# Optimization experiments

Hardware: AMD Instinct MI355X
Metric: run time of the kernel (lower is better)

Reference implementation:

```python
import jax, jax.numpy as jnp
import numpy as np

B, S, D, N = 4, 1024, 1024, 32768


def setup_inputs() -> dict:
    key = jax.random.key(0)
    ks = jax.random.split(key, 6)
    return {
        "x": jax.random.normal(ks[0], (B, S, D), jnp.float32),
        "h": jax.random.normal(ks[1], (B, S, D), jnp.float32),
        "emb": jax.random.normal(ks[2], (N, D), jnp.float32),
        "tau_offset": jax.random.normal(ks[3], (B, S, 1), jnp.float32) * 0.1,
        "w_read": jax.random.normal(ks[4], (N, D), jnp.float32) * 0.02,
        "w_write": jax.random.normal(ks[5], (N, D), jnp.float32) * 0.02,
        "n_chunks": 8,
    }


def _srw_chunked(x, h, emb_unit, tau_offset, w_read, w_write, n_chunks):
    """Two chunked passes over neuron pool: (1) online score stats, (2) STE
    threshold-gated read->write projection with cost-weighted normalization."""
    Bb, Ss, Dd = x.shape
    Nn = emb_unit.shape[0]
    cs = Nn // n_chunks
    h_bf = h.astype(jnp.bfloat16)
    x_bf = x.astype(jnp.bfloat16)
    emb_bf = emb_unit.astype(jnp.bfloat16)
    read_bf = w_read.astype(jnp.bfloat16)
    write_bf = w_write.astype(jnp.bfloat16)
    z1 = jnp.zeros((Bb, Ss, 1))

    @jax.checkpoint
    def stats_step(carry, i):
        s_sum, sq_sum, ns_sum, ns_sq = carry
        s = i * cs
        ec = jax.lax.dynamic_slice_in_dim(emb_bf, s, cs, axis=0)
        scores = h_bf @ ec.T  # [B,S,cs]
        s_sum = s_sum + scores.sum(axis=-1, keepdims=True).astype(jnp.float32)
        sq_sum = sq_sum + (scores.astype(jnp.float32) ** 2).sum(axis=-1, keepdims=True)
        per_neuron_score = scores.astype(jnp.float32).mean(axis=(0, 1))
        ns_sum = ns_sum + per_neuron_score.sum()
        ns_sq = ns_sq + (per_neuron_score ** 2).sum()
        return ((s_sum, sq_sum, ns_sum, ns_sq), None)

    z_bs1 = jnp.zeros((Bb, Ss, 1))
    z_scalar = jnp.float32(0.0)
    (s_sum, sq_sum, ns_sum, ns_sq), _ = jax.lax.scan(
        stats_step, (z_bs1, z_bs1, z_scalar, z_scalar), jnp.arange(n_chunks))
    s_mean = s_sum / Nn
    s_std = jnp.sqrt(sq_sum / Nn - s_mean ** 2) + 1e-08
    tau = s_mean + tau_offset * s_std
    mean_score = ns_sum / Nn
    var_score = ns_sq / Nn - mean_score ** 2
    score_lb = var_score / (mean_score ** 2 + var_score + 0.01)

    @jax.checkpoint
    def gate_srw_step(carry, i):
        out, total_weighted_cost, total_gate_max, total_active = carry
        s = i * cs
        ec = jax.lax.dynamic_slice_in_dim(emb_bf, s, cs, axis=0)
        rc = jax.lax.dynamic_slice_in_dim(read_bf, s, cs, axis=0)
        wc = jax.lax.dynamic_slice_in_dim(write_bf, s, cs, axis=0)
        rc = rc / (jnp.linalg.norm(rc, axis=-1, keepdims=True) + 1e-08)
        wc = wc / (jnp.linalg.norm(wc, axis=-1, keepdims=True) + 1e-08)
        scores = h_bf @ ec.T
        raw = scores.astype(jnp.float32) - tau
        gate_hard = (raw > 0).astype(jnp.float32)
        sig = jax.nn.sigmoid(raw / s_std)
        gate = gate_hard + sig - jax.lax.stop_gradient(sig)  # straight-through
        gate_bf = gate.astype(jnp.bfloat16)
        xr = x_bf @ rc.T                     # read projection [B,S,cs]
        c_out = (gate_bf * xr @ wc).astype(jnp.float32)  # write projection
        xr_f32 = xr.astype(jnp.float32)
        cost = jax.lax.stop_gradient(xr_f32 ** 2)
        chunk_weighted = (sig * cost).sum(axis=-1, keepdims=True)
        chunk_active = gate_hard.sum(axis=-1, keepdims=True)
        return ((out + c_out,
                 total_weighted_cost + chunk_weighted,
                 jnp.maximum(total_gate_max, gate_hard.max(axis=-1, keepdims=True)),
                 total_active + chunk_active), None)

    (raw_out, total_weighted_cost, total_gate_max, total_active), _ = jax.lax.scan(
        gate_srw_step,
        (jnp.zeros((Bb, Ss, Dd), dtype=jnp.float32), z1,
         jnp.full((Bb, Ss, 1), -1000000000.0), z1),
        jnp.arange(n_chunks))
    den = jnp.sqrt(total_weighted_cost + 1e-06)
    den = jnp.maximum(den, 0.001)
    out = (raw_out / den).astype(jnp.bfloat16)
    score_std_out = s_std.mean()
    es_out = total_weighted_cost.mean()
    active_n_mean = total_active.mean()
    score_mean_out = s_mean.mean()
    return (out.astype(jnp.float32), total_active / Nn, total_gate_max, score_lb,
            score_std_out, es_out, active_n_mean, score_mean_out)


def reference(x, h, emb, tau_offset, w_read, w_write, n_chunks):
    # Caller normalizes the embedding pool to unit rows before the chunked pass.
    emb_unit = emb / (jnp.linalg.norm(emb, axis=-1, keepdims=True) + 1e-08)
    return _srw_chunked(x, h, emb_unit, tau_offset, w_read, w_write, n_chunks)
```

## Files before the change

### kernel.cpp

```cpp
#include <hip/hip_runtime.h>
#include <stdint.h>

#define M_TOT 4096
#define D_DIM 1024
#define N_NEUR 32768
#define NCHUNK 8
#define CS 4096

typedef float f32x4 __attribute__((ext_vector_type(4)));
typedef __bf16 bf16x8 __attribute__((ext_vector_type(8)));
typedef unsigned short u16;
typedef unsigned int u32;
typedef u16 u16x8 __attribute__((ext_vector_type(8)));
typedef u16 u16x4 __attribute__((ext_vector_type(4)));

__device__ __forceinline__ u16 f2bf(float f) {
    u32 u = __builtin_bit_cast(u32, f);
    u = (u + 0x7FFFu + ((u >> 16) & 1u)) >> 16;
    return (u16)u;
}
__device__ __forceinline__ float bf2f(u16 h) {
    u32 u = ((u32)h) << 16;
    return __builtin_bit_cast(float, u);
}
__device__ __forceinline__ u32 pack2(float a, float b, float s) {
    return (u32)f2bf(a * s) | ((u32)f2bf(b * s) << 16);
}

typedef __attribute__((address_space(1))) const u32 as1_u32;
typedef __attribute__((address_space(3))) u32 as3_u32;
__device__ __forceinline__ void gload16(const void* g, void* l) {
    __builtin_amdgcn_global_load_lds((as1_u32*)g, (as3_u32*)l, 16, 0, 0);
}

#define MFMA(a, b, c) __builtin_amdgcn_mfma_f32_16x16x32_bf16((a), (b), (c), 0, 0, 0)

#define GEMM128_BODY(ABASE, ASTR, BBASE, BSTR, KLEN)                                  \
    __shared__ u16 LDS[17408];                                                        \
    u16* Al = LDS;                                                                    \
    u16* Bl = LDS + 4096;                                                             \
    const int t = threadIdx.x, lane = t & 63, w = t >> 6;                             \
    const int wr = w >> 1, wc = w & 1, l15 = lane & 15, lg = lane >> 4;               \
    f32x4 acc[4][4] = {};                                                             \
    {                                                                                 \
        const int rb = lane >> 2, cl = (lane & 3) * 8;                                \
        const int seg0 = w * 2;                                                       \
        const size_t ro0 = (size_t)(seg0 * 16 + rb);                                  \
        const u16* pa0 = (ABASE) + ((size_t)bm * 128 + ro0) * (ASTR) + cl;            \
        const u16* pb0 = (BBASE) + ((size_t)bn * 128 + ro0) * (BSTR) + cl;            \
        const u16* pa1 = pa0 + (size_t)16 * (ASTR);                                   \
        const u16* pb1 = pb0 + (size_t)16 * (BSTR);                                   \
        u16* la0 = Al + seg0 * 512;                                                   \
        u16* lb0 = Bl + seg0 * 512;                                                   \
        for (int k0 = 0; k0 < (KLEN); k0 += 32) {                                     \
            __syncthreads();                                                          \
            gload16(pa0 + k0, la0);                                                   \
            gload16(pa1 + k0, la0 + 512);                                             \
            gload16(pb0 + k0, lb0);                                                   \
            gload16(pb1 + k0, lb0 + 512);                                             \
            __syncthreads();                                                          \
            bf16x8 afr[4], bfr[4];                                                    \
            _Pragma("unroll") for (int m = 0; m < 4; m++)                             \
                afr[m] = *(const bf16x8*)&Al[(wr * 64 + m * 16 + l15) * 32 + lg * 8]; \
            _Pragma("unroll") for (int n = 0; n < 4; n++)                             \
                bfr[n] = *(const bf16x8*)&Bl[(wc * 64 + n * 16 + l15) * 32 + lg * 8]; \
            _Pragma("unroll") for (int m = 0; m < 4; m++)                             \
                _Pragma("unroll") for (int n = 0; n < 4; n++)                         \
                    acc[m][n] = MFMA(afr[m], bfr[n], acc[m][n]);                      \
        }                                                                             \
    }

#define RESTAGE_TO_LDS(VALS)                                                          \
    __syncthreads();                                                                  \
    _Pragma("unroll") for (int m = 0; m < 4; m++)                                     \
        _Pragma("unroll") for (int rr = 0; rr < 4; rr++)                              \
            _Pragma("unroll") for (int n = 0; n < 4; n++) {                           \
                int lrow = wr * 64 + m * 16 + lg * 4 + rr;                            \
                LDS[lrow * 136 + wc * 64 + n * 16 + l15] = (VALS);                    \
            }                                                                         \
    __syncthreads();

#define RESTAGE_U16_TILE(VALS, DSTBASE, DSTSTRIDE, COLBASE)                           \
    {                                                                                 \
        RESTAGE_TO_LDS(VALS)                                                          \
        int row_ = t >> 2, c0_ = (t & 3) * 32;                                        \
        _Pragma("unroll") for (int p = 0; p < 2; p++) {                               \
            int lrow = p * 64 + row_;                                                 \
            u16* dst_ = (DSTBASE) + (size_t)(bm * 128 + lrow) * (DSTSTRIDE) +         \
                        (COLBASE) + c0_;                                              \
            const u16* srcl_ = &LDS[lrow * 136 + c0_];                                \
            _Pragma("unroll") for (int j = 0; j < 4; j++)                             \
                *(u16x8*)(dst_ + j * 8) = *(const u16x8*)(srcl_ + j * 8);             \
        }                                                                             \
    }

__global__ __launch_bounds__(256) void k_cvt(const float* __restrict__ h,
                                             const float* __restrict__ x,
                                             u16* __restrict__ hb, u16* __restrict__ xb) {
    size_t i = ((size_t)blockIdx.x * 256 + threadIdx.x) * 4;
    float4 v = *(const float4*)(h + i);
    uint2 o;
    o.x = pack2(v.x, v.y, 1.0f);
    o.y = pack2(v.z, v.w, 1.0f);
    *(uint2*)(hb + i) = o;
    v = *(const float4*)(x + i);
    o.x = pack2(v.x, v.y, 1.0f);
    o.y = pack2(v.z, v.w, 1.0f);
    *(uint2*)(xb + i) = o;
}

__global__ __launch_bounds__(256) void k_cvt_ern3(const float* __restrict__ emb,
                                                  const float* __restrict__ wrd,
                                                  const float* __restrict__ ww,
                                                  u16* __restrict__ ebf, u16* __restrict__ rbf,
                                                  float* __restrict__ sw) {
    int t = threadIdx.x, lane = t & 63, wv = t >> 6;
    int row = blockIdx.x * 4 + wv;
    int which = blockIdx.y;
    const float* srcm = which == 0 ? emb : (which == 1 ? wrd : ww);
    const float4* src = (const float4*)(srcm + (size_t)row * D_DIM);
    float4 v[4];
    float ss = 0.f;
#pragma unroll
    for (int j = 0; j < 4; j++) {
        v[j] = src[j * 64 + lane];
        if (which == 0) {
            ss += v[j].x * v[j].x + v[j].y * v[j].y + v[j].z * v[j].z + v[j].w * v[j].w;
        } else {
            float a = bf2f(f2bf(v[j].x)), b = bf2f(f2bf(v[j].y));
            float c = bf2f(f2bf(v[j].z)), d = bf2f(f2bf(v[j].w));
            ss += a * a + b * b + c * c + d * d;
        }
    }
#pragma unroll
    for (int s = 1; s < 64; s <<= 1) ss += __shfl_xor(ss, s);
    float sc = 1.0f / (sqrtf(ss) + 1e-8f);
    if (which == 2) {
        if (lane == 0) sw[row] = sc;
        return;
    }
    uint2* dst = (uint2*)((which == 0 ? ebf : rbf) + (size_t)row * D_DIM);
#pragma unroll
    for (int j = 0; j < 4; j++) {
        uint2 o;
        o.x = pack2(v[j].x, v[j].y, sc);
        o.y = pack2(v[j].z, v[j].w, sc);
        dst[j * 64 + lane] = o;
    }
}

__global__ __launch_bounds__(256) void k_cvt_e_norm(const float* __restrict__ emb,
                                                    int cbase, u16* __restrict__ ebf) {
    int t = threadIdx.x, lane = t & 63, wv = t >> 6;
    int row = blockIdx.x * 4 + wv;
    const float4* src = (const float4*)(emb + (size_t)(cbase + row) * D_DIM);
    float4 v[4];
    float ss = 0.f;
#pragma unroll
    for (int j = 0; j < 4; j++) {
        v[j] = src[j * 64 + lane];
        ss += v[j].x * v[j].x + v[j].y * v[j].y + v[j].z * v[j].z + v[j].w * v[j].w;
    }
#pragma unroll
    for (int s = 1; s < 64; s <<= 1) ss += __shfl_xor(ss, s);
    float es = 1.0f / (sqrtf(ss) + 1e-8f);
    uint2* dst = (uint2*)(ebf + (size_t)row * D_DIM);
#pragma unroll
    for (int j = 0; j < 4; j++) {
        uint2 o;
        o.x = pack2(v[j].x, v[j].y, es);
        o.y = pack2(v[j].z, v[j].w, es);
        dst[j * 64 + lane] = o;
    }
}

__global__ __launch_bounds__(256) void k_cvt_r_norm(const float* __restrict__ wrd,
                                                    int cbase, u16* __restrict__ rbf) {
    int t = threadIdx.x, lane = t & 63, wv = t >> 6;
    int row = blockIdx.x * 4 + wv;
    const float4* src = (const float4*)(wrd + (size_t)(cbase + row) * D_DIM);
    float4 v[4];
    float ss = 0.f;
#pragma unroll
    for (int j = 0; j < 4; j++) {
        v[j] = src[j * 64 + lane];
        float a = bf2f(f2bf(v[j].x)), b = bf2f(f2bf(v[j].y));
        float c = bf2f(f2bf(v[j].z)), d = bf2f(f2bf(v[j].w));
        ss += a * a + b * b + c * c + d * d;
    }
#pragma unroll
    for (int s = 1; s < 64; s <<= 1) ss += __shfl_xor(ss, s);
    float rs = 1.0f / (sqrtf(ss) + 1e-8f);
    uint2* dst = (uint2*)(rbf + (size_t)row * D_DIM);
#pragma unroll
    for (int j = 0; j < 4; j++) {
        uint2 o;
        o.x = pack2(v[j].x, v[j].y, rs);
        o.y = pack2(v[j].z, v[j].w, rs);
        dst[j * 64 + lane] = o;
    }
}

__global__ __launch_bounds__(256) void k_sw(const float* __restrict__ ww, float* sw) {
    int t = threadIdx.x, lane = t & 63, wv = t >> 6;
    int row = blockIdx.x * 4 + wv;
    const float4* src = (const float4*)(ww + (size_t)row * D_DIM);
    float ss = 0.f;
#pragma unroll
    for (int j = 0; j < 4; j++) {
        float4 v = src[j * 64 + lane];
        float a = bf2f(f2bf(v.x)), b = bf2f(f2bf(v.y));
        float c = bf2f(f2bf(v.z)), d = bf2f(f2bf(v.w));
        ss += a * a + b * b + c * c + d * d;
    }
#pragma unroll
    for (int s = 1; s < 64; s <<= 1) ss += __shfl_xor(ss, s);
    if (lane == 0) sw[row] = 1.0f / (sqrtf(ss) + 1e-8f);
}

__global__ __launch_bounds__(256) void k_tww(const float* __restrict__ ww,
                                             const float* __restrict__ sw,
                                             int cbase, u16* __restrict__ wwT, int dstr) {
    __shared__ u16 tile[64][80];
    int kt = blockIdx.x * 64;
    int dt = blockIdx.y * 64;
    int t = threadIdx.x;
    int kk = t >> 4;
    int dd = (t & 15) * 4;
#pragma unroll
    for (int i = 0; i < 4; i++) {
        int krow = kk + i * 16;
        int kg = cbase + kt + krow;
        float s = sw[kg];
        float4 v = *(const float4*)(ww + (size_t)kg * D_DIM + dt + dd);
        tile[dd + 0][krow] = f2bf(v.x * s);
        tile[dd + 1][krow] = f2bf(v.y * s);
        tile[dd + 2][krow] = f2bf(v.z * s);
        tile[dd + 3][krow] = f2bf(v.w * s);
    }
    __syncthreads();
    int dd2 = t >> 2;
    int kk2 = (t & 3) * 16;
    uint4 o0 = *(const uint4*)&tile[dd2][kk2];
    uint4 o1 = *(const uint4*)&tile[dd2][kk2 + 8];
    u16* dst = wwT + (size_t)(dt + dd2) * dstr + kt + kk2;
    *(uint4*)dst = o0;
    *(uint4*)(dst + 8) = o1;
}

__global__ __launch_bounds__(256) void k_pass1(const u16* __restrict__ hb,
                                               const u16* __restrict__ ebf, int cbase,
                                               float* rowsum, float* rowsq, float* colsum,
                                               u16* __restrict__ sb, int sstr) {
    int bm = blockIdx.x, bn = blockIdx.y;
    GEMM128_BODY(hb, D_DIM, ebf, D_DIM, D_DIM)
    float csv[4] = {0.f, 0.f, 0.f, 0.f};
#pragma unroll
    for (int m = 0; m < 4; m++)
#pragma unroll
        for (int rr = 0; rr < 4; rr++)
#pragma unroll
            for (int n = 0; n < 4; n++) csv[n] += bf2f(f2bf(acc[m][n][rr]));
#pragma unroll
    for (int n = 0; n < 4; n++) {
        float cv = csv[n];
        cv += __shfl_xor(cv, 16);
        cv += __shfl_xor(cv, 32);
        if (lg == 0) {
            int ng = cbase + bn * 128 + wc * 64 + n * 16 + l15;
            atomicAdd(&colsum[ng], cv);
        }
    }
    RESTAGE_TO_LDS(f2bf(acc[m][n][rr]))
    int row_ = t >> 2, c0_ = (t & 3) * 32;
#pragma unroll
    for (int p = 0; p < 2; p++) {
        int lrow = p * 64 + row_;
        int grow = bm * 128 + lrow;
        float rs = 0.f, rq = 0.f;
        u16* dst = sb ? (sb + (size_t)grow * sstr + cbase + bn * 128 + c0_) : (u16*)nullptr;
#pragma unroll
        for (int j = 0; j < 4; j++) {
            u16x8 v = *(const u16x8*)&LDS[lrow * 136 + c0_ + j * 8];
            if (dst) *(u16x8*)(dst + j * 8) = v;
#pragma unroll
            for (int q = 0; q < 8; q++) {
                float sv = bf2f(v[q]);
                rs += sv;
                rq += sv * sv;
            }
        }
        rs += __shfl_xor(rs, 1);
        rq += __shfl_xor(rq, 1);
        rs += __shfl_xor(rs, 2);
        rq += __shfl_xor(rq, 2);
        if ((lane & 3) == 0) {
            atomicAdd(&rowsum[grow], rs);
            atomicAdd(&rowsq[grow], rq);
        }
    }
}

__global__ __launch_bounds__(256) void k_ns(const float* __restrict__ colsum, float* scal) {
    int i = blockIdx.x * 256 + threadIdx.x;
    float pm = colsum[i] * (1.0f / 4096.0f);
    float s1 = pm, s2 = pm * pm;
#pragma unroll
    for (int x = 1; x < 64; x <<= 1) {
        s1 += __shfl_xor(s1, x);
        s2 += __shfl_xor(s2, x);
    }
    __shared__ float sh[2][4];
    int w = threadIdx.x >> 6;
    if ((threadIdx.x & 63) == 0) { sh[0][w] = s1; sh[1][w] = s2; }
    __syncthreads();
    if (threadIdx.x == 0) {
        atomicAdd(&scal[0], sh[0][0] + sh[0][1] + sh[0][2] + sh[0][3]);
        atomicAdd(&scal[1], sh[1][0] + sh[1][1] + sh[1][2] + sh[1][3]);
    }
}

__global__ __launch_bounds__(256) void k_tau(const float* __restrict__ rowsum,
                                             const float* __restrict__ rowsq,
                                             const float* __restrict__ tau_off,
                                             float* tau, float* invstd, float* smean, float* sstd) {
    int i = blockIdx.x * 256 + threadIdx.x;
    float sm = rowsum[i] * (1.0f / 32768.0f);
    float var = rowsq[i] * (1.0f / 32768.0f) - sm * sm;
    float sd = sqrtf(var) + 1e-8f;
    smean[i] = sm;
    sstd[i] = sd;
    invstd[i] = 1.0f / sd;
    tau[i] = sm + tau_off[i] * sd;
}

__global__ __launch_bounds__(256) void k_xr_gate_all(const u16* __restrict__ xb,
                                                     const u16* __restrict__ rbf,
                                                     u16* __restrict__ sbP,
                                                     const float* __restrict__ tau,
                                                     const float* __restrict__ invstd,
                                                     float* twc, float* act) {
    int bm = blockIdx.x, bn = blockIdx.y;
    const int tt = threadIdx.x;
    const int prow = tt >> 2, pc0 = (tt & 3) * 32;
    u16x8 sv_pre[2][4];
#pragma unroll
    for (int p = 0; p < 2; p++) {
        int grow = bm * 128 + p * 64 + prow;
        const u16* src = sbP + (size_t)grow * N_NEUR + bn * 128 + pc0;
#pragma unroll
        for (int j = 0; j < 4; j++) sv_pre[p][j] = *(const u16x8*)(src + j * 8);
    }
    GEMM128_BODY(xb, D_DIM, rbf, D_DIM, D_DIM)
    RESTAGE_TO_LDS(f2bf(acc[m][n][rr]))
#pragma unroll
    for (int p = 0; p < 2; p++) {
        int lrow = p * 64 + prow;
        int grow = bm * 128 + lrow;
        float tl = tau[grow], il = invstd[grow];
        float wsum = 0.f, cnt = 0.f;
        u16* gptr = sbP + (size_t)grow * N_NEUR + bn * 128 + pc0;
#pragma unroll
        for (int j = 0; j < 4; j++) {
            u16x8 xr8 = *(const u16x8*)&LDS[lrow * 136 + pc0 + j * 8];
            u16x8 sv8 = sv_pre[p][j];
            u16x8 o;
#pragma unroll
            for (int q = 0; q < 8; q++) {
                float xf = bf2f(xr8[q]);
                float raw = bf2f(sv8[q]) - tl;
                float sig = 1.0f / (1.0f + __expf(-raw * il));
                bool g = raw > 0.0f;
                wsum += sig * xf * xf;
                cnt += g ? 1.0f : 0.0f;
                o[q] = g ? xr8[q] : (u16)0;
            }
            *(u16x8*)(gptr + j * 8) = o;
        }
        wsum += __shfl_xor(wsum, 1);
        cnt += __shfl_xor(cnt, 1);
        wsum += __shfl_xor(wsum, 2);
        cnt += __shfl_xor(cnt, 2);
        if ((lane & 3) == 0) {
            atomicAdd(&twc[grow], wsum);
            atomicAdd(&act[grow], cnt);
        }
    }
}

__global__ __launch_bounds__(256) void k_pass2b_all(const u16* __restrict__ sbP,
                                                    const u16* __restrict__ wwT,
                                                    u16* __restrict__ part) {
    int bm = blockIdx.x;
    int bn = blockIdx.y;
    int zz = blockIdx.z;
    const u16* Pz = sbP + (size_t)zz * CS;
    const u16* Wz = wwT + (size_t)zz * CS;
    u16* pz = part + (size_t)zz * M_TOT * D_DIM;
    GEMM128_BODY(Pz, N_NEUR, Wz, N_NEUR, CS)
    RESTAGE_U16_TILE(f2bf(acc[m][n][rr]), pz, D_DIM, bn * 128)
}

__global__ __launch_bounds__(256) void k_norm_comb(const u16* __restrict__ part,
                                                   const float* __restrict__ twc,
                                                   const float* __restrict__ act,
                                                   float* __restrict__ out0,
                                                   float* out1, float* out2) {
    int row = blockIdx.x;
    float den = sqrtf(twc[row] + 1e-6f);
    den = fmaxf(den, 0.001f);
    float inv = 1.0f / den;
    size_t base = (size_t)row * D_DIM + threadIdx.x * 4;
    float s0 = 0.f, s1 = 0.f, s2 = 0.f, s3 = 0.f;
#pragma unroll
    for (int c = 0; c < NCHUNK; c++) {
        u16x4 v = *(const u16x4*)(part + (size_t)c * M_TOT * D_DIM + base);
        s0 += bf2f(v[0]);
        s1 += bf2f(v[1]);
        s2 += bf2f(v[2]);
        s3 += bf2f(v[3]);
    }
    float4 o;
    o.x = bf2f(f2bf(s0 * inv));
    o.y = bf2f(f2bf(s1 * inv));
    o.z = bf2f(f2bf(s2 * inv));
    o.w = bf2f(f2bf(s3 * inv));
    *(float4*)(out0 + base) = o;
    if (threadIdx.x == 0) {
        out1[row] = act[row] * (1.0f / 32768.0f);
        out2[row] = act[row] > 0.0f ? 1.0f : 0.0f;
    }
}

__global__ __launch_bounds__(256) void k_xr_plain(const u16* __restrict__ xb,
                                                  const u16* __restrict__ rbf,
                                                  u16* __restrict__ P) {
    int bm = blockIdx.x, bn = blockIdx.y;
    GEMM128_BODY(xb, D_DIM, rbf, D_DIM, D_DIM)
    RESTAGE_U16_TILE(f2bf(acc[m][n][rr]), P, CS, bn * 128)
}

__global__ __launch_bounds__(256) void k_gate_gemm(const u16* __restrict__ hb,
                                                   const u16* __restrict__ ebf,
                                                   const float* __restrict__ tau,
                                                   const float* __restrict__ invstd,
                                                   u16* __restrict__ P, float* twc, float* act) {
    int bm = blockIdx.x, bn = blockIdx.y;
    GEMM128_BODY(hb, D_DIM, ebf, D_DIM, D_DIM)
#pragma unroll
    for (int m = 0; m < 4; m++) {
#pragma unroll
        for (int rr = 0; rr < 4; rr++) {
            int mg = bm * 128 + wr * 64 + m * 16 + lg * 4 + rr;
            float tl = tau[mg], il = invstd[mg];
            float wsum = 0.f, cnt = 0.f;
#pragma unroll
            for (int n = 0; n < 4; n++) {
                int ngl = bn * 128 + wc * 64 + n * 16 + l15;
                float sv = bf2f(f2bf(acc[m][n][rr]));
                float raw = sv - tl;
                u16 xrb = P[(size_t)mg * CS + ngl];
                float xf = bf2f(xrb);
                float sig = 1.0f / (1.0f + __expf(-raw * il));
                bool g = raw > 0.0f;
                wsum += sig * xf * xf;
                cnt += g ? 1.0f : 0.0f;
                P[(size_t)mg * CS + ngl] = g ? xrb : (u16)0;
            }
#pragma unroll
            for (int x = 1; x < 16; x <<= 1) {
                wsum += __shfl_xor(wsum, x);
                cnt += __shfl_xor(cnt, x);
            }
            if (l15 == 0) {
                atomicAdd(&twc[mg], wsum);
                atomicAdd(&act[mg], cnt);
            }
        }
    }
}

__global__ __launch_bounds__(256) void k_pass2b(const u16* __restrict__ P,
                                                const u16* __restrict__ wwT, int bstr,
                                                float* __restrict__ out) {
    int bm = blockIdx.x;
    int bn = blockIdx.y;
    GEMM128_BODY(P, CS, wwT, bstr, CS)
#pragma unroll
    for (int m = 0; m < 4; m++)
#pragma unroll
        for (int n = 0; n < 4; n++)
#pragma unroll
            for (int rr = 0; rr < 4; rr++) {
                int mg = bm * 128 + wr * 64 + m * 16 + lg * 4 + rr;
                int dg = bn * 128 + wc * 64 + n * 16 + l15;
                out[(size_t)mg * D_DIM + dg] += bf2f(f2bf(acc[m][n][rr]));
            }
}

__global__ __launch_bounds__(256) void k_norm_f(float* __restrict__ out,
                                                const float* __restrict__ twc,
                                                const float* __restrict__ act,
                                                float* out1, float* out2) {
    int row = blockIdx.x;
    float den = sqrtf(twc[row] + 1e-6f);
    den = fmaxf(den, 0.001f);
    float inv = 1.0f / den;
    float* p = out + (size_t)row * D_DIM;
    int i = threadIdx.x * 4;
    float4 v = *(float4*)(p + i);
    v.x = bf2f(f2bf(v.x * inv));
    v.y = bf2f(f2bf(v.y * inv));
    v.z = bf2f(f2bf(v.z * inv));
    v.w = bf2f(f2bf(v.w * inv));
    *(float4*)(p + i) = v;
    if (threadIdx.x == 0) {
        out1[row] = act[row] * (1.0f / 32768.0f);
        out2[row] = act[row] > 0.0f ? 1.0f : 0.0f;
    }
}

__global__ __launch_bounds__(256) void k_scalars(const float* __restrict__ smean,
                                                 const float* __restrict__ sstd,
                                                 const float* __restrict__ twc,
                                                 const float* __restrict__ act,
                                                 const float* __restrict__ scal,
                                                 float* outS) {
    float a = 0.f, b = 0.f, c = 0.f, d = 0.f;
    for (int i = threadIdx.x; i < 4096; i += 256) {
        a += smean[i];
        b += sstd[i];
        c += twc[i];
        d += act[i];
    }
#pragma unroll
    for (int x = 1; x < 64; x <<= 1) {
        a += __shfl_xor(a, x);
        b += __shfl_xor(b, x);
        c += __shfl_xor(c, x);
        d += __shfl_xor(d, x);
    }
    __shared__ float sh[4][4];
    int w = threadIdx.x >> 6;
    if ((threadIdx.x & 63) == 0) { sh[0][w] = a; sh[1][w] = b; sh[2][w] = c; sh[3][w] = d; }
    __syncthreads();
    if (threadIdx.x == 0) {
        float ma = sh[0][0] + sh[0][1] + sh[0][2] + sh[0][3];
        float mb = sh[1][0] + sh[1][1] + sh[1][2] + sh[1][3];
        float mc = sh[2][0] + sh[2][1] + sh[2][2] + sh[2][3];
        float md = sh[3][0] + sh[3][1] + sh[3][2] + sh[3][3];
        float mean_score = scal[0] * (1.0f / 32768.0f);
        float var_score = scal[1] * (1.0f / 32768.0f) - mean_score * mean_score;
        outS[0] = var_score / (mean_score * mean_score + var_score + 0.01f);
        outS[1] = mb * (1.0f / 4096.0f);
        outS[2] = mc * (1.0f / 4096.0f);
        outS[3] = md * (1.0f / 4096.0f);
        outS[4] = ma * (1.0f / 4096.0f);
    }
}

static constexpr size_t OFF_HB     = 0;
static constexpr size_t OFF_XB     = 8388608;
static constexpr size_t OFF_P      = 16777216;
static constexpr size_t OFF_EBF    = 50331648;
static constexpr size_t OFF_RBF    = 117440512;
static constexpr size_t OFF_WWT    = 184549376;
static constexpr size_t OFF_SW     = 251658240;
static constexpr size_t OFF_ROWSUM = 251789312;
static constexpr size_t OFF_ROWSQ  = 251805696;
static constexpr size_t OFF_COLSUM = 251822080;
static constexpr size_t OFF_TAU    = 251953152;
static constexpr size_t OFF_INVSTD = 251969536;
static constexpr size_t OFF_SMEAN  = 251985920;
static constexpr size_t OFF_SSTD   = 252002304;
static constexpr size_t OFF_TWC    = 252018688;
static constexpr size_t OFF_ACT    = 252035072;
static constexpr size_t OFF_SCAL   = 252051456;
static constexpr size_t STATS_END  = 252051520;
static constexpr size_t ZERO_LEN   = STATS_END - OFF_ROWSUM;
static constexpr size_t OFF_SB     = 252706816;
static constexpr size_t FULL_END   = OFF_SB + (size_t)M_TOT * N_NEUR * 2;
static constexpr size_t OFF_PART   = OFF_EBF;

extern "C" void kernel_launch(void* const* d_in, const int* in_sizes, int n_in,
                              void* d_out, int out_size, void* d_ws, size_t ws_size,
                              hipStream_t stream) {
    const float* x = (const float*)d_in[0];
    const float* h = (const float*)d_in[1];
    const float* emb = (const float*)d_in[2];
    const float* tau_off = (const float*)d_in[3];
    const float* w_read = (const float*)d_in[4];
    const float* w_write = (const float*)d_in[5];
    char* ws = (char*)d_ws;
    u16* hb = (u16*)(ws + OFF_HB);
    u16* xb = (u16*)(ws + OFF_XB);
    u16* P = (u16*)(ws + OFF_P);
    u16* ebf = (u16*)(ws + OFF_EBF);
    u16* rbf = (u16*)(ws + OFF_RBF);
    u16* wwT = (u16*)(ws + OFF_WWT);
    float* sw = (float*)(ws + OFF_SW);
    float* rowsum = (float*)(ws + OFF_ROWSUM);
    float* rowsq = (float*)(ws + OFF_ROWSQ);
    float* colsum = (float*)(ws + OFF_COLSUM);
    float* tau = (float*)(ws + OFF_TAU);
    float* invstd = (float*)(ws + OFF_INVSTD);
    float* smean = (float*)(ws + OFF_SMEAN);
    float* sstd = (float*)(ws + OFF_SSTD);
    float* twc = (float*)(ws + OFF_TWC);
    float* act = (float*)(ws + OFF_ACT);
    float* scal = (float*)(ws + OFF_SCAL);
    u16* part = (u16*)(ws + OFF_PART);
    const bool fullA = ws_size >= FULL_END;
    u16* sbP = fullA ? (u16*)(ws + OFF_SB) : (u16*)nullptr;

    float* out0 = (float*)d_out;
    float* out1 = out0 + (size_t)M_TOT * D_DIM;
    float* out2 = out1 + M_TOT;
    float* outS = out2 + M_TOT;

    hipMemsetAsync(ws + OFF_ROWSUM, 0, ZERO_LEN, stream);

    k_cvt<<<4096, 256, 0, stream>>>(h, x, hb, xb);

    if (fullA) {
        k_cvt_ern3<<<dim3(N_NEUR / 4, 3), 256, 0, stream>>>(emb, w_read, w_write,
                                                            ebf, rbf, sw);
        k_tww<<<dim3(N_NEUR / 64, 16), 256, 0, stream>>>(w_write, sw, 0, wwT, N_NEUR);
        k_pass1<<<dim3(32, 256), 256, 0, stream>>>(hb, ebf, 0, rowsum, rowsq, colsum,
                                                   sbP, N_NEUR);
        k_ns<<<128, 256, 0, stream>>>(colsum, scal);
        k_tau<<<16, 256, 0, stream>>>(rowsum, rowsq, tau_off, tau, invstd, smean, sstd);
        k_xr_gate_all<<<dim3(32, 256), 256, 0, stream>>>(xb, rbf, sbP, tau, invstd, twc, act);
        k_pass2b_all<<<dim3(32, 8, 8), 256, 0, stream>>>(sbP, wwT, part);
        k_norm_comb<<<4096, 256, 0, stream>>>(part, twc, act, out0, out1, out2);
    } else {
        hipMemsetAsync(d_out, 0, (size_t)M_TOT * D_DIM * 4, stream);
        k_sw<<<N_NEUR / 4, 256, 0, stream>>>(w_write, sw);
        for (int c = 0; c < NCHUNK; c++) {
            k_cvt_e_norm<<<CS / 4, 256, 0, stream>>>(emb, c * CS, ebf);
            k_pass1<<<dim3(32, 32), 256, 0, stream>>>(hb, ebf, c * CS, rowsum, rowsq, colsum,
                                                      (u16*)nullptr, 0);
        }
        k_ns<<<128, 256, 0, stream>>>(colsum, scal);
        k_tau<<<16, 256, 0, stream>>>(rowsum, rowsq, tau_off, tau, invstd, smean, sstd);
        for (int c = 0; c < NCHUNK; c++) {
            k_cvt_e_norm<<<CS / 4, 256, 0, stream>>>(emb, c * CS, ebf);
            k_cvt_r_norm<<<CS / 4, 256, 0, stream>>>(w_read, c * CS, rbf);
            k_tww<<<dim3(CS / 64, 16), 256, 0, stream>>>(w_write, sw, c * CS, wwT, CS);
            k_xr_plain<<<dim3(32, 32), 256, 0, stream>>>(xb, rbf, P);
            k_gate_gemm<<<dim3(32, 32), 256, 0, stream>>>(hb, ebf, tau, invstd, P, twc, act);
            k_pass2b<<<dim3(32, 8), 256, 0, stream>>>(P, wwT, CS, out0);
        }
        k_norm_f<<<4096, 256, 0, stream>>>(out0, twc, act, out1, out2);
    }
    k_scalars<<<1, 256, 0, stream>>>(smean, sstd, twc, act, scal, outS);
}
```

Before: 1.509 ms.

## Double-buffer LDS tiles in GEMM main loop to overlap loads with MFMA

Splits the shared-memory staging area into two halves. The next K-slice is prefetched with global_load_lds while the current slice feeds the MFMAs, and explicit vmcnt waits plus raw s_barrier replace the two __syncthreads per iteration. The goal is to hide global-load latency behind compute in every GEMM built on this macro. The cost is reliance on hand-written waitcnt and barrier ordering, which could be fragile if the compiler reorders LDS reads.

```diff
diff --git a/kernel.cpp b/kernel.cpp
--- a/kernel.cpp
+++ b/kernel.cpp
@@ -37,36 +37,45 @@
 
 #define GEMM128_BODY(ABASE, ASTR, BBASE, BSTR, KLEN)                                  \
     __shared__ u16 LDS[17408];                                                        \
-    u16* Al = LDS;                                                                    \
-    u16* Bl = LDS + 4096;                                                             \
     const int t = threadIdx.x, lane = t & 63, w = t >> 6;                             \
     const int wr = w >> 1, wc = w & 1, l15 = lane & 15, lg = lane >> 4;               \
     f32x4 acc[4][4] = {};                                                             \
     {                                                                                 \
+        const int seg0 = w * 2;                                                       \
         const int rb = lane >> 2, cl = (lane & 3) * 8;                                \
-        const int seg0 = w * 2;                                                       \
         const size_t ro0 = (size_t)(seg0 * 16 + rb);                                  \
         const u16* pa0 = (ABASE) + ((size_t)bm * 128 + ro0) * (ASTR) + cl;            \
         const u16* pb0 = (BBASE) + ((size_t)bn * 128 + ro0) * (BSTR) + cl;            \
         const u16* pa1 = pa0 + (size_t)16 * (ASTR);                                   \
         const u16* pb1 = pb0 + (size_t)16 * (BSTR);                                   \
-        u16* la0 = Al + seg0 * 512;                                                   \
-        u16* lb0 = Bl + seg0 * 512;                                                   \
+        gload16(pa0, LDS + seg0 * 512);                                               \
+        gload16(pa1, LDS + seg0 * 512 + 512);                                         \
+        gload16(pb0, LDS + 4096 + seg0 * 512);                                        \
+        gload16(pb1, LDS + 4096 + seg0 * 512 + 512);                                  \
         for (int k0 = 0; k0 < (KLEN); k0 += 32) {                                     \
-            __syncthreads();                                                          \
-            gload16(pa0 + k0, la0);                                                   \
-            gload16(pa1 + k0, la0 + 512);                                             \
-            gload16(pb0 + k0, lb0);                                                   \
-            gload16(pb1 + k0, lb0 + 512);                                             \
-            __syncthreads();                                                          \
+            const int co = ((k0 >> 5) & 1) * 8192;                                    \
+            const int no = co ^ 8192;                                                 \
+            if (k0 + 32 < (KLEN)) {                                                   \
+                gload16(pa0 + k0 + 32, LDS + no + seg0 * 512);                        \
+                gload16(pa1 + k0 + 32, LDS + no + seg0 * 512 + 512);                  \
+                gload16(pb0 + k0 + 32, LDS + no + 4096 + seg0 * 512);                 \
+                gload16(pb1 + k0 + 32, LDS + no + 4096 + seg0 * 512 + 512);           \
+                asm volatile("s_waitcnt vmcnt(4)" ::: "memory");                      \
+            } else {                                                                  \
+                asm volatile("s_waitcnt vmcnt(0)" ::: "memory");                      \
+            }                                                                         \
+            __builtin_amdgcn_s_barrier();                                             \
             bf16x8 afr[4], bfr[4];                                                    \
             _Pragma("unroll") for (int m = 0; m < 4; m++)                             \
-                afr[m] = *(const bf16x8*)&Al[(wr * 64 + m * 16 + l15) * 32 + lg * 8]; \
+                afr[m] = *(const bf16x8*)&LDS[co + (wr * 64 + m * 16 + l15) * 32 +    \
+                                              lg * 8];                                \
             _Pragma("unroll") for (int n = 0; n < 4; n++)                             \
-                bfr[n] = *(const bf16x8*)&Bl[(wc * 64 + n * 16 + l15) * 32 + lg * 8]; \
+                bfr[n] = *(const bf16x8*)&LDS[co + 4096 +                             \
+                                              (wc * 64 + n * 16 + l15) * 32 + lg * 8];\
             _Pragma("unroll") for (int m = 0; m < 4; m++)                             \
                 _Pragma("unroll") for (int n = 0; n < 4; n++)                         \
                     acc[m][n] = MFMA(afr[m], bfr[n], acc[m][n]);                      \
+            __builtin_amdgcn_s_barrier();                                             \
         }                                                                             \
     }
 
```

After: 1.480 ms. About the same (-1.9%).
